# Kernel tuning notes

Measured on AMD Instinct MI355X. Metric: run time of the kernel, lower is better.

Reference implementation:

```python
import jax, jax.numpy as jnp
import numpy as np
import math

B, S, E, HEAD = 4, 2048, 1024, 64  # num_heads=16 -> head_size = 1024//16


def setup_inputs() -> dict:
    key = jax.random.key(0)
    kx, kp, kq, kk, kv = jax.random.split(key, 5)
    std = math.sqrt(2.0 / (E + HEAD))
    return {
        "x": jax.random.normal(kx, (B, S, E), dtype=jnp.float32),
        "padding_mask": jax.random.randint(kp, (B, S), 0, 2, dtype=jnp.int32),
        "Wq": jax.random.normal(kq, (HEAD, E), dtype=jnp.float32) * std,
        "Wk": jax.random.normal(kk, (HEAD, E), dtype=jnp.float32) * std,
        "Wv": jax.random.normal(kv, (HEAD, E), dtype=jnp.float32) * std,
    }


def reference(x, padding_mask, Wq, Wk, Wv):
    # q,k,v: [B,S,head] via Linear (x @ W.T, no bias)
    q = jnp.einsum("bse,he->bsh", x, Wq)
    k = jnp.einsum("bse,he->bsh", x, Wk)
    v = jnp.einsum("bse,he->bsh", x, Wv)
    scores = jnp.einsum("bqh,bkh->bqk", q, k)  # [B,S,S]
    seq = x.shape[1]
    causal = jnp.tril(jnp.ones((seq, seq), dtype=jnp.float32))  # [S,S]
    mask = causal[None, :, :] * padding_mask.astype(jnp.float32)[:, None, :]  # [B,S,S]
    scores = jnp.where(mask == 0, jnp.float32(-1e9), scores)
    head_size = k.shape[-1]
    attn = jax.nn.softmax(scores / jnp.sqrt(jnp.float32(head_size)), axis=-1)
    return jnp.einsum("bqk,bkh->bqh", attn, v)
```

## Files before the change

kernel.cpp:

```cpp
#include <hip/hip_runtime.h>
#include <hip/hip_bf16.h>
#include <math.h>

#define B_ 4
#define S_ 2048
#define E_ 1024
#define H_ 64
#define NQT 32
#define SPLITS 8
#define TPS 4
#define SENT (-1.25e8f)

typedef short bf16x8 __attribute__((ext_vector_type(8)));
typedef float f32x4 __attribute__((ext_vector_type(4)));
typedef unsigned short U16;
typedef U16 u16x8 __attribute__((ext_vector_type(8)));
typedef U16 u16x4 __attribute__((ext_vector_type(4)));

__device__ __forceinline__ U16 f2bf(float f){
    unsigned u = __builtin_bit_cast(unsigned, f);
    u += 0x7fffu + ((u >> 16) & 1u);
    return (U16)(u >> 16);
}
__device__ __forceinline__ float bf2f(U16 h){
    return __builtin_bit_cast(float, ((unsigned)h) << 16);
}
#define MFMA16(a,b,c) __builtin_amdgcn_mfma_f32_16x16x32_bf16((a),(b),(c),0,0,0)

typedef const __attribute__((address_space(1))) void GvPtr;
typedef __attribute__((address_space(3))) void LdsPtr;
__device__ __forceinline__ void gload_lds16(const void* g, void* l){
    __builtin_amdgcn_global_load_lds((GvPtr*)g, (LdsPtr*)l, 16, 0, 0);
}

__global__ __launch_bounds__(256) void prep_w(
    const float* __restrict__ Wq, const float* __restrict__ Wk,
    const float* __restrict__ Wv, U16* __restrict__ Whi, U16* __restrict__ Wlo)
{
    int i4 = (blockIdx.x*256 + threadIdx.x) * 4;
    int c = i4 >> 16, rem = i4 & 65535;
    const float* src = (c==0) ? Wq : (c==1) ? Wk : Wv;
    float4 v = *(const float4*)(src + rem);
    float a[4] = {v.x, v.y, v.z, v.w};
    u16x4 hv, lv;
    #pragma unroll
    for (int j=0;j<4;j++){ U16 h = f2bf(a[j]); hv[j]=h; lv[j]=f2bf(a[j]-bf2f(h)); }
    *(u16x4*)(Whi + i4) = hv;
    *(u16x4*)(Wlo + i4) = lv;
}

__global__ __launch_bounds__(256) void qkv_kernel(
    const float* __restrict__ x, const U16* __restrict__ Whi_g,
    const U16* __restrict__ Wlo_g,
    U16* __restrict__ Qhi, U16* __restrict__ Qlo,
    U16* __restrict__ Khi, U16* __restrict__ Klo, U16* __restrict__ Vt)
{
    __shared__ __align__(16) U16 Ah[2][32*64], Al[2][32*64];
    const int m0 = blockIdx.x * 32;
    const int tid = threadIdx.x, lane = tid & 63, wv = tid >> 6;
    const int l15 = lane & 15, quad = lane >> 4;
    const int arow = tid >> 3, ag = tid & 7;

    f32x4 acc[3][2];
    #pragma unroll
    for (int c=0;c<3;c++)
    #pragma unroll
    for (int mt=0;mt<2;mt++) acc[c][mt] = f32x4{0.f,0.f,0.f,0.f};

    {
        const float* xs = x + (size_t)(m0 + arow)*E_ + ag*8;
        float4 xa = ((const float4*)xs)[0], xb = ((const float4*)xs)[1];
        float vv[8] = {xa.x,xa.y,xa.z,xa.w,xb.x,xb.y,xb.z,xb.w};
        u16x8 hv, lv;
        #pragma unroll
        for (int j=0;j<8;j++){ U16 h = f2bf(vv[j]); hv[j]=h; lv[j]=f2bf(vv[j]-bf2f(h)); }
        ((u16x8*)Ah[0])[arow*8 + ag] = hv;
        ((u16x8*)Al[0])[arow*8 + ag] = lv;
    }
    __syncthreads();

    int p = 0;
    for (int k0 = 0; k0 < E_; k0 += 64) {
        float4 xa, xb;
        const bool have = (k0 + 64 < E_);
        if (have) {
            const float* xs = x + (size_t)(m0 + arow)*E_ + k0 + 64 + ag*8;
            xa = ((const float4*)xs)[0]; xb = ((const float4*)xs)[1];
        }
        bf16x8 bh[3][2], bl[3][2];
        #pragma unroll
        for (int c=0;c<3;c++)
        #pragma unroll
        for (int kk=0;kk<2;kk++){
            const size_t wo = (size_t)c*65536 + (size_t)(wv*16 + l15)*E_ + k0 + kk*32 + quad*8;
            bh[c][kk] = *(const bf16x8*)(Whi_g + wo);
            bl[c][kk] = *(const bf16x8*)(Wlo_g + wo);
        }
        #pragma unroll
        for (int kk=0;kk<2;kk++){
            #pragma unroll
            for (int mt=0;mt<2;mt++){
                const int ai = (mt*16 + l15)*8 + kk*4 + quad;
                bf16x8 ah = ((const bf16x8*)Ah[p])[ai];
                bf16x8 al = ((const bf16x8*)Al[p])[ai];
                #pragma unroll
                for (int c=0;c<3;c++){
                    acc[c][mt] = MFMA16(ah, bh[c][kk], acc[c][mt]);
                    acc[c][mt] = MFMA16(ah, bl[c][kk], acc[c][mt]);
                    acc[c][mt] = MFMA16(al, bh[c][kk], acc[c][mt]);
                }
            }
        }
        if (have) {
            float vv[8] = {xa.x,xa.y,xa.z,xa.w,xb.x,xb.y,xb.z,xb.w};
            u16x8 hv, lv;
            #pragma unroll
            for (int j=0;j<8;j++){ U16 h = f2bf(vv[j]); hv[j]=h; lv[j]=f2bf(vv[j]-bf2f(h)); }
            ((u16x8*)Ah[p^1])[arow*8 + ag] = hv;
            ((u16x8*)Al[p^1])[arow*8 + ag] = lv;
        }
        __syncthreads();
        p ^= 1;
    }

    const int h = wv*16 + l15;
    #pragma unroll
    for (int mt=0;mt<2;mt++){
        const int row = m0 + mt*16 + quad*4;
        #pragma unroll
        for (int r=0;r<4;r++){
            float vq = acc[0][mt][r]; U16 hq = f2bf(vq);
            Qhi[(size_t)(row+r)*H_ + h] = hq;
            Qlo[(size_t)(row+r)*H_ + h] = f2bf(vq - bf2f(hq));
            float vk = acc[1][mt][r]; U16 hk = f2bf(vk);
            Khi[(size_t)(row+r)*H_ + h] = hk;
            Klo[(size_t)(row+r)*H_ + h] = f2bf(vk - bf2f(hk));
        }
        const int b = row >> 11, s0 = row & (S_-1);
        u16x4 pk;
        #pragma unroll
        for (int r=0;r<4;r++) pk[r] = f2bf(acc[2][mt][r]);
        *(u16x4*)(Vt + ((size_t)b*H_ + h)*S_ + s0) = pk;
    }
}

__global__ __launch_bounds__(256) void attn_kernel(
    const U16* __restrict__ Qhi, const U16* __restrict__ Qlo,
    const U16* __restrict__ Khi, const U16* __restrict__ Klo,
    const U16* __restrict__ Vt, const int* __restrict__ pad,
    float* __restrict__ Opart, float* __restrict__ mpart, float* __restrict__ lpart)
{
    const int qt = blockIdx.x, b = blockIdx.y, sp = blockIdx.z;
    const int t0 = sp * TPS;
    if (t0 > qt) return;
    const int t1 = min(t0 + TPS, qt + 1);

    __shared__ __align__(16) U16 KtH[64*64], KtL[64*64], Vts[64*64];
    __shared__ __align__(16) U16 Ps[4][16*80];

    const int tid = threadIdx.x, lane = tid & 63, wv = tid >> 6;
    const int l15 = lane & 15, quad = lane >> 4;

    const size_t qrow = (size_t)b*S_ + qt*64 + wv*16 + l15;
    bf16x8 aqh0 = *(const bf16x8*)(Qhi + qrow*H_ + quad*8);
    bf16x8 aqh1 = *(const bf16x8*)(Qhi + qrow*H_ + 32 + quad*8);
    bf16x8 aql0 = *(const bf16x8*)(Qlo + qrow*H_ + quad*8);
    bf16x8 aql1 = *(const bf16x8*)(Qlo + qrow*H_ + 32 + quad*8);

    float m_i = -INFINITY, l_i = 0.f;
    f32x4 o[4];
    #pragma unroll
    for (int i=0;i<4;i++) o[i] = f32x4{0.f,0.f,0.f,0.f};
    const int qg = qt*64 + wv*16 + l15;
    U16* Pw = &Ps[wv][0];

    for (int t = t0; t < t1; ++t) {
        const int kb = t * 64;
        __syncthreads();
        {
            const U16* kh = Khi + ((size_t)b*S_ + kb)*H_;
            const U16* kl = Klo + ((size_t)b*S_ + kb)*H_;
            #pragma unroll
            for (int ch=0; ch<2; ++ch){
                const int sb = wv*128 + ch*64;
                const int slot = sb + lane;
                gload_lds16(kh + (size_t)slot*8, (U16*)KtH + sb*8);
                gload_lds16(kl + (size_t)slot*8, (U16*)KtL + sb*8);
                const int vrow = slot >> 3, vg = slot & 7;
                gload_lds16(Vt + ((size_t)b*H_ + vrow)*S_ + kb + vg*8, (U16*)Vts + sb*8);
            }
        }
        const unsigned long long pm = __ballot(pad[(size_t)b*S_ + kb + lane] != 0);
        __syncthreads();

        f32x4 z[4];
        #pragma unroll
        for (int nt=0; nt<4; nt++){
            const int kr = (nt*16 + l15)*8;
            bf16x8 kh0 = ((const bf16x8*)KtH)[kr + quad];
            bf16x8 kh1 = ((const bf16x8*)KtH)[kr + 4 + quad];
            bf16x8 kl0 = ((const bf16x8*)KtL)[kr + quad];
            bf16x8 kl1 = ((const bf16x8*)KtL)[kr + 4 + quad];
            f32x4 zz = f32x4{0.f,0.f,0.f,0.f};
            zz = MFMA16(kh0, aqh0, zz);
            zz = MFMA16(kh1, aqh1, zz);
            zz = MFMA16(kh0, aql0, zz);
            zz = MFMA16(kh1, aql1, zz);
            zz = MFMA16(kl0, aqh0, zz);
            zz = MFMA16(kl1, aqh1, zz);
            z[nt] = zz;
        }
        float rmax = -INFINITY;
        #pragma unroll
        for (int nt=0; nt<4; nt++){
            const int rel = qg - kb - nt*16 - quad*4;
            const unsigned mb = (unsigned)(pm >> (nt*16 + quad*4)) & 0xFu;
            #pragma unroll
            for (int r=0;r<4;r++){
                const bool ok = (r <= rel) && ((mb >> r) & 1u);
                const float v = ok ? z[nt][r]*0.125f : SENT;
                z[nt][r] = v;
                rmax = fmaxf(rmax, v);
            }
        }
        rmax = fmaxf(rmax, __shfl_xor(rmax, 16));
        rmax = fmaxf(rmax, __shfl_xor(rmax, 32));
        const float mn = fmaxf(m_i, rmax);
        const float alpha = __expf(m_i - mn);
        m_i = mn;
        float rsum = 0.f;
        #pragma unroll
        for (int nt=0; nt<4; nt++)
        #pragma unroll
        for (int r=0;r<4;r++){
            const float pv = __expf(z[nt][r] - mn);
            z[nt][r] = pv;
            rsum += pv;
        }
        rsum += __shfl_xor(rsum, 16);
        rsum += __shfl_xor(rsum, 32);
        l_i = l_i*alpha + rsum;
        #pragma unroll
        for (int nt=0; nt<4; nt++)
        #pragma unroll
        for (int r=0;r<4;r++) o[nt][r] *= alpha;

        #pragma unroll
        for (int nt=0; nt<4; nt++){
            u16x4 pk;
            #pragma unroll
            for (int r=0;r<4;r++) pk[r] = f2bf(z[nt][r]);
            *(u16x4*)(Pw + l15*80 + nt*16 + quad*4) = pk;
        }
        #pragma unroll
        for (int ks=0; ks<2; ks++){
            bf16x8 bp = *(const bf16x8*)(Pw + l15*80 + ks*32 + quad*8);
            #pragma unroll
            for (int nt=0; nt<4; nt++){
                bf16x8 av = ((const bf16x8*)Vts)[(nt*16 + l15)*8 + ks*4 + quad];
                o[nt] = MFMA16(av, bp, o[nt]);
            }
        }
    }
    const size_t rbase = ((size_t)((b*NQT + qt)*SPLITS + sp))*64 + wv*16 + l15;
    if (quad == 0) { mpart[rbase] = m_i; lpart[rbase] = l_i; }
    #pragma unroll
    for (int nt=0; nt<4; nt++)
        *((f32x4*)(Opart + rbase*H_ + nt*16 + quad*4)) = o[nt];
}

__global__ __launch_bounds__(256) void combine_kernel(
    const float* __restrict__ Opart, const float* __restrict__ mpart,
    const float* __restrict__ lpart, const U16* __restrict__ Vt,
    float* __restrict__ out)
{
    const int idx = blockIdx.x*256 + threadIdx.x;
    const int h = idx & 63;
    const int q = (idx >> 6) & (S_-1);
    const int b = idx >> 17;
    const int qt = q >> 6, r = q & 63;
    const int ns = (qt >> 2) + 1;
    const size_t rb = ((size_t)(b*NQT + qt)*SPLITS)*64 + r;
    float M = -INFINITY;
    for (int s2=0; s2<ns; s2++) M = fmaxf(M, mpart[rb + (size_t)s2*64]);
    float res;
    if (M == SENT) {
        const U16* vsrc = Vt + ((size_t)b*H_ + h)*S_;
        float sm = 0.f;
        for (int s=0; s<S_; ++s) sm += bf2f(vsrc[s]);
        res = sm * (1.f/(float)S_);
    } else {
        float L = 0.f, accv = 0.f;
        for (int s2=0; s2<ns; s2++){
            const float mi = mpart[rb + (size_t)s2*64];
            const float w = __expf(mi - M);
            L    += w * lpart[rb + (size_t)s2*64];
            accv += w * Opart[(rb + (size_t)s2*64)*H_ + h];
        }
        res = accv / L;
    }
    out[idx] = res;
}

extern "C" void kernel_launch(void* const* d_in, const int* in_sizes, int n_in,
                              void* d_out, int out_size, void* d_ws, size_t ws_size,
                              hipStream_t stream)
{
    (void)in_sizes; (void)n_in; (void)out_size; (void)ws_size;
    const float* x  = (const float*)d_in[0];
    const int* pad  = (const int*)d_in[1];
    const float* Wq = (const float*)d_in[2];
    const float* Wk = (const float*)d_in[3];
    const float* Wv = (const float*)d_in[4];
    float* out = (float*)d_out;
    char* ws = (char*)d_ws;
    const size_t MB = 1u << 20;
    U16* Whi = (U16*)(ws);
    U16* Wlo = (U16*)(ws + 393216);
    U16* Qhi = (U16*)(ws + 1*MB);
    U16* Qlo = (U16*)(ws + 2*MB);
    U16* Khi = (U16*)(ws + 3*MB);
    U16* Klo = (U16*)(ws + 4*MB);
    U16* Vt  = (U16*)(ws + 5*MB);
    float* Opart = (float*)(ws + 6*MB);
    float* mpart = (float*)(ws + 22*MB);
    float* lpart = (float*)(ws + 22*MB + (1u<<18));

    prep_w<<<dim3(192), 256, 0, stream>>>(Wq, Wk, Wv, Whi, Wlo);
    qkv_kernel<<<dim3(256), 256, 0, stream>>>(x, Whi, Wlo, Qhi, Qlo, Khi, Klo, Vt);
    attn_kernel<<<dim3(NQT, B_, SPLITS), 256, 0, stream>>>(Qhi, Qlo, Khi, Klo, Vt, pad,
                                                           Opart, mpart, lpart);
    combine_kernel<<<dim3((B_*S_*H_)/256), 256, 0, stream>>>(Opart, mpart, lpart, Vt, out);
}
```

Before: 164.4 us.

## Double-buffer attention K/V tiles, swizzle LDS, and split-K the QKV projection

The attention kernel now double-buffers the K-hi, K-lo and V tiles in LDS. It issues the async global-to-LDS loads and the padding-mask load for the next key tile before computing on the current one, and drops one barrier per iteration. All LDS tiles use an XOR swizzle of the 16-byte column groups to reduce bank conflicts on the MFMA operand reads. The QKV projection moves to 512 threads and splits the K dimension in half across wave groups, with register prefetch of the next weight slice and a shared-memory reduction at the end. The aim is to hide global load latency and raise occupancy, at the cost of more LDS and more registers per block.

Result: faster. 152.8 us (-7.0%).

```diff
diff --git a/kernel.cpp b/kernel.cpp
--- a/kernel.cpp
+++ b/kernel.cpp
@@ -49,17 +49,21 @@
     *(u16x4*)(Wlo + i4) = lv;
 }
 
-__global__ __launch_bounds__(256) void qkv_kernel(
+__global__ __launch_bounds__(512) void qkv_kernel(
     const float* __restrict__ x, const U16* __restrict__ Whi_g,
     const U16* __restrict__ Wlo_g,
     U16* __restrict__ Qhi, U16* __restrict__ Qlo,
     U16* __restrict__ Khi, U16* __restrict__ Klo, U16* __restrict__ Vt)
 {
-    __shared__ __align__(16) U16 Ah[2][32*64], Al[2][32*64];
+    __shared__ __align__(16) U16 XH[2][2][2048], XL[2][2][2048];
+    __shared__ __align__(16) float Red[4*64*28];
     const int m0 = blockIdx.x * 32;
     const int tid = threadIdx.x, lane = tid & 63, wv = tid >> 6;
     const int l15 = lane & 15, quad = lane >> 4;
-    const int arow = tid >> 3, ag = tid & 7;
+    const int hs = (wv & 3) * 16;
+    const int kh = wv >> 2;
+    const int p2 = tid >> 8;
+    const int rr = (tid >> 3) & 31, ag = tid & 7;
 
     f32x4 acc[3][2];
     #pragma unroll
@@ -67,80 +71,107 @@
     #pragma unroll
     for (int mt=0;mt<2;mt++) acc[c][mt] = f32x4{0.f,0.f,0.f,0.f};
 
-    {
-        const float* xs = x + (size_t)(m0 + arow)*E_ + ag*8;
-        float4 xa = ((const float4*)xs)[0], xb = ((const float4*)xs)[1];
-        float vv[8] = {xa.x,xa.y,xa.z,xa.w,xb.x,xb.y,xb.z,xb.w};
+    const float* xrow = x + (size_t)(m0 + rr)*E_ + (size_t)p2*512 + ag*8;
+
+    auto cvwrite = [&](int buf, float4 a, float4 b2){
+        float vv[8] = {a.x,a.y,a.z,a.w,b2.x,b2.y,b2.z,b2.w};
         u16x8 hv, lv;
         #pragma unroll
         for (int j=0;j<8;j++){ U16 h = f2bf(vv[j]); hv[j]=h; lv[j]=f2bf(vv[j]-bf2f(h)); }
-        ((u16x8*)Ah[0])[arow*8 + ag] = hv;
-        ((u16x8*)Al[0])[arow*8 + ag] = lv;
-    }
+        const int idx = rr*8 + (ag ^ (rr & 7));
+        ((u16x8*)XH[buf][p2])[idx] = hv;
+        ((u16x8*)XL[buf][p2])[idx] = lv;
+    };
+
+    const size_t wbase = (size_t)(hs + l15)*E_ + (size_t)kh*512 + quad*8;
+    bf16x8 bhc[3][2], blc[3][2], bhn[3][2], bln[3][2];
+    auto loadW = [&](int it, bf16x8 (*bh)[2], bf16x8 (*bl)[2]){
+        #pragma unroll
+        for (int c=0;c<3;c++)
+        #pragma unroll
+        for (int kk=0;kk<2;kk++){
+            const size_t o = (size_t)c*65536 + wbase + it*64 + kk*32;
+            bh[c][kk] = *(const bf16x8*)(Whi_g + o);
+            bl[c][kk] = *(const bf16x8*)(Wlo_g + o);
+        }
+    };
+
+    {   float4 xa = ((const float4*)xrow)[0], xb = ((const float4*)xrow)[1];
+        cvwrite(0, xa, xb); }
+    loadW(0, bhc, blc);
     __syncthreads();
 
     int p = 0;
-    for (int k0 = 0; k0 < E_; k0 += 64) {
+    for (int it = 0; it < 8; ++it) {
+        const bool have = (it < 7);
         float4 xa, xb;
-        const bool have = (k0 + 64 < E_);
         if (have) {
-            const float* xs = x + (size_t)(m0 + arow)*E_ + k0 + 64 + ag*8;
+            const float* xs = xrow + (it+1)*64;
             xa = ((const float4*)xs)[0]; xb = ((const float4*)xs)[1];
-        }
-        bf16x8 bh[3][2], bl[3][2];
+            loadW(it+1, bhn, bln);
+        }
+        #pragma unroll
+        for (int kk=0;kk<2;kk++)
+        #pragma unroll
+        for (int mt=0;mt<2;mt++){
+            const int row = mt*16 + l15;
+            const int idx = row*8 + ((kk*4+quad) ^ (l15 & 7));
+            bf16x8 ah = ((const bf16x8*)XH[p][kh])[idx];
+            bf16x8 al = ((const bf16x8*)XL[p][kh])[idx];
+            #pragma unroll
+            for (int c=0;c<3;c++){
+                acc[c][mt] = MFMA16(ah, bhc[c][kk], acc[c][mt]);
+                acc[c][mt] = MFMA16(ah, blc[c][kk], acc[c][mt]);
+                acc[c][mt] = MFMA16(al, bhc[c][kk], acc[c][mt]);
+            }
+        }
+        if (have) cvwrite(p^1, xa, xb);
+        __syncthreads();
+        if (have) {
+            #pragma unroll
+            for (int c=0;c<3;c++)
+            #pragma unroll
+            for (int kk=0;kk<2;kk++){ bhc[c][kk]=bhn[c][kk]; blc[c][kk]=bln[c][kk]; }
+        }
+        p ^= 1;
+    }
+
+    if (kh == 1) {
+        float* rp = &Red[((wv&3)*64 + lane)*28];
         #pragma unroll
         for (int c=0;c<3;c++)
         #pragma unroll
-        for (int kk=0;kk<2;kk++){
-            const size_t wo = (size_t)c*65536 + (size_t)(wv*16 + l15)*E_ + k0 + kk*32 + quad*8;
-            bh[c][kk] = *(const bf16x8*)(Whi_g + wo);
-            bl[c][kk] = *(const bf16x8*)(Wlo_g + wo);
-        }
-        #pragma unroll
-        for (int kk=0;kk<2;kk++){
-            #pragma unroll
-            for (int mt=0;mt<2;mt++){
-                const int ai = (mt*16 + l15)*8 + kk*4 + quad;
-                bf16x8 ah = ((const bf16x8*)Ah[p])[ai];
-                bf16x8 al = ((const bf16x8*)Al[p])[ai];
-                #pragma unroll
-                for (int c=0;c<3;c++){
-                    acc[c][mt] = MFMA16(ah, bh[c][kk], acc[c][mt]);
-                    acc[c][mt] = MFMA16(ah, bl[c][kk], acc[c][mt]);
-                    acc[c][mt] = MFMA16(al, bh[c][kk], acc[c][mt]);
-                }
+        for (int mt=0;mt<2;mt++)
+            *(f32x4*)(rp + (c*2+mt)*4) = acc[c][mt];
+    }
+    __syncthreads();
+    if (kh == 0) {
+        const float* rp = &Red[((wv&3)*64 + lane)*28];
+        #pragma unroll
+        for (int c=0;c<3;c++)
+        #pragma unroll
+        for (int mt=0;mt<2;mt++)
+            acc[c][mt] += *(const f32x4*)(rp + (c*2+mt)*4);
+
+        const int h = hs + l15;
+        #pragma unroll
+        for (int mt=0;mt<2;mt++){
+            const int row = m0 + mt*16 + quad*4;
+            #pragma unroll
+            for (int r=0;r<4;r++){
+                float vq = acc[0][mt][r]; U16 hq = f2bf(vq);
+                Qhi[(size_t)(row+r)*H_ + h] = hq;
+                Qlo[(size_t)(row+r)*H_ + h] = f2bf(vq - bf2f(hq));
+                float vk = acc[1][mt][r]; U16 hk = f2bf(vk);
+                Khi[(size_t)(row+r)*H_ + h] = hk;
+                Klo[(size_t)(row+r)*H_ + h] = f2bf(vk - bf2f(hk));
             }
-        }
-        if (have) {
-            float vv[8] = {xa.x,xa.y,xa.z,xa.w,xb.x,xb.y,xb.z,xb.w};
-            u16x8 hv, lv;
-            #pragma unroll
-            for (int j=0;j<8;j++){ U16 h = f2bf(vv[j]); hv[j]=h; lv[j]=f2bf(vv[j]-bf2f(h)); }
-            ((u16x8*)Ah[p^1])[arow*8 + ag] = hv;
-            ((u16x8*)Al[p^1])[arow*8 + ag] = lv;
-        }
-        __syncthreads();
-        p ^= 1;
-    }
-
-    const int h = wv*16 + l15;
-    #pragma unroll
-    for (int mt=0;mt<2;mt++){
-        const int row = m0 + mt*16 + quad*4;
-        #pragma unroll
-        for (int r=0;r<4;r++){
-            float vq = acc[0][mt][r]; U16 hq = f2bf(vq);
-            Qhi[(size_t)(row+r)*H_ + h] = hq;
-            Qlo[(size_t)(row+r)*H_ + h] = f2bf(vq - bf2f(hq));
-            float vk = acc[1][mt][r]; U16 hk = f2bf(vk);
-            Khi[(size_t)(row+r)*H_ + h] = hk;
-            Klo[(size_t)(row+r)*H_ + h] = f2bf(vk - bf2f(hk));
-        }
-        const int b = row >> 11, s0 = row & (S_-1);
-        u16x4 pk;
-        #pragma unroll
-        for (int r=0;r<4;r++) pk[r] = f2bf(acc[2][mt][r]);
-        *(u16x4*)(Vt + ((size_t)b*H_ + h)*S_ + s0) = pk;
+            const int b = row >> 11, s0 = row & (S_-1);
+            u16x4 pk;
+            #pragma unroll
+            for (int r=0;r<4;r++) pk[r] = f2bf(acc[2][mt][r]);
+            *(u16x4*)(Vt + ((size_t)b*H_ + h)*S_ + s0) = pk;
+        }
     }
 }
 
@@ -155,11 +186,26 @@
     if (t0 > qt) return;
     const int t1 = min(t0 + TPS, qt + 1);
 
-    __shared__ __align__(16) U16 KtH[64*64], KtL[64*64], Vts[64*64];
+    __shared__ __align__(16) U16 KtH[2][64*64], KtL[2][64*64], Vts[2][64*64];
     __shared__ __align__(16) U16 Ps[4][16*80];
 
     const int tid = threadIdx.x, lane = tid & 63, wv = tid >> 6;
     const int l15 = lane & 15, quad = lane >> 4;
+
+    auto stage = [&](int t, int bb){
+        const int kb2 = t * 64;
+        const U16* khp = Khi + ((size_t)b*S_ + kb2)*H_;
+        const U16* klp = Klo + ((size_t)b*S_ + kb2)*H_;
+        #pragma unroll
+        for (int ch=0; ch<2; ++ch){
+            const int sb = wv*128 + ch*64;
+            const int u = sb + lane;
+            const int row = u >> 3, g = u & 7, gs = g ^ (row & 7);
+            gload_lds16(khp + (size_t)row*H_ + gs*8, KtH[bb] + sb*8);
+            gload_lds16(klp + (size_t)row*H_ + gs*8, KtL[bb] + sb*8);
+            gload_lds16(Vt + ((size_t)b*H_ + row)*S_ + kb2 + gs*8, Vts[bb] + sb*8);
+        }
+    };
 
     const size_t qrow = (size_t)b*S_ + qt*64 + wv*16 + l15;
     bf16x8 aqh0 = *(const bf16x8*)(Qhi + qrow*H_ + quad*8);
@@ -174,33 +220,29 @@
     const int qg = qt*64 + wv*16 + l15;
     U16* Pw = &Ps[wv][0];
 
-    for (int t = t0; t < t1; ++t) {
+    stage(t0, 0);
+    int pv = pad[(size_t)b*S_ + t0*64 + lane];
+
+    int p = 0;
+    for (int t = t0; t < t1; ++t, p ^= 1) {
+        __syncthreads();
+        int pvn = 0;
+        if (t + 1 < t1) {
+            stage(t+1, p^1);
+            pvn = pad[(size_t)b*S_ + (t+1)*64 + lane];
+        }
+        const unsigned long long pm = __ballot(pv != 0);
         const int kb = t * 64;
-        __syncthreads();
-        {
-            const U16* kh = Khi + ((size_t)b*S_ + kb)*H_;
-            const U16* kl = Klo + ((size_t)b*S_ + kb)*H_;
-            #pragma unroll
-            for (int ch=0; ch<2; ++ch){
-                const int sb = wv*128 + ch*64;
-                const int slot = sb + lane;
-                gload_lds16(kh + (size_t)slot*8, (U16*)KtH + sb*8);
-                gload_lds16(kl + (size_t)slot*8, (U16*)KtL + sb*8);
-                const int vrow = slot >> 3, vg = slot & 7;
-                gload_lds16(Vt + ((size_t)b*H_ + vrow)*S_ + kb + vg*8, (U16*)Vts + sb*8);
-            }
-        }
-        const unsigned long long pm = __ballot(pad[(size_t)b*S_ + kb + lane] != 0);
-        __syncthreads();
+        const int sw = l15 & 7;
 
         f32x4 z[4];
         #pragma unroll
         for (int nt=0; nt<4; nt++){
             const int kr = (nt*16 + l15)*8;
-            bf16x8 kh0 = ((const bf16x8*)KtH)[kr + quad];
-            bf16x8 kh1 = ((const bf16x8*)KtH)[kr + 4 + quad];
-            bf16x8 kl0 = ((const bf16x8*)KtL)[kr + quad];
-            bf16x8 kl1 = ((const bf16x8*)KtL)[kr + 4 + quad];
+            bf16x8 kh0 = ((const bf16x8*)KtH[p])[kr + (quad ^ sw)];
+            bf16x8 kh1 = ((const bf16x8*)KtH[p])[kr + ((4+quad) ^ sw)];
+            bf16x8 kl0 = ((const bf16x8*)KtL[p])[kr + (quad ^ sw)];
+            bf16x8 kl1 = ((const bf16x8*)KtL[p])[kr + ((4+quad) ^ sw)];
             f32x4 zz = f32x4{0.f,0.f,0.f,0.f};
             zz = MFMA16(kh0, aqh0, zz);
             zz = MFMA16(kh1, aqh1, zz);
@@ -233,9 +275,9 @@
         for (int nt=0; nt<4; nt++)
         #pragma unroll
         for (int r=0;r<4;r++){
-            const float pv = __expf(z[nt][r] - mn);
-            z[nt][r] = pv;
-            rsum += pv;
+            const float pe = __expf(z[nt][r] - mn);
+            z[nt][r] = pe;
+            rsum += pe;
         }
         rsum += __shfl_xor(rsum, 16);
         rsum += __shfl_xor(rsum, 32);
@@ -257,10 +299,11 @@
             bf16x8 bp = *(const bf16x8*)(Pw + l15*80 + ks*32 + quad*8);
             #pragma unroll
             for (int nt=0; nt<4; nt++){
-                bf16x8 av = ((const bf16x8*)Vts)[(nt*16 + l15)*8 + ks*4 + quad];
+                bf16x8 av = ((const bf16x8*)Vts[p])[(nt*16 + l15)*8 + ((ks*4+quad) ^ sw)];
                 o[nt] = MFMA16(av, bp, o[nt]);
             }
         }
+        pv = pvn;
     }
     const size_t rbase = ((size_t)((b*NQT + qt)*SPLITS + sp))*64 + wv*16 + l15;
     if (quad == 0) { mpart[rbase] = m_i; lpart[rbase] = l_i; }
@@ -327,7 +370,7 @@
     float* lpart = (float*)(ws + 22*MB + (1u<<18));
 
     prep_w<<<dim3(192), 256, 0, stream>>>(Wq, Wk, Wv, Whi, Wlo);
-    qkv_kernel<<<dim3(256), 256, 0, stream>>>(x, Whi, Wlo, Qhi, Qlo, Khi, Klo, Vt);
+    qkv_kernel<<<dim3(256), 512, 0, stream>>>(x, Whi, Wlo, Qhi, Qlo, Khi, Klo, Vt);
     attn_kernel<<<dim3(NQT, B_, SPLITS), 256, 0, stream>>>(Qhi, Qlo, Khi, Klo, Vt, pad,
                                                            Opart, mpart, lpart);
     combine_kernel<<<dim3((B_*S_*H_)/256), 256, 0, stream>>>(Opart, mpart, lpart, Vt, out);
```

## Split QKV projection over K across waves and swizzle attention LDS tiles

Applied to the files above, without the earlier changes.

The QKV projection kernel is restructured so that each block handles 64 rows for a single Q/K/V component, with the grid spanning components. Each of the four waves covers a quarter of the E dimension, loading x directly from global memory into registers with double buffering, and the partial sums are reduced through shared memory. This removes the per-step LDS staging and barriers and raises parallelism, at the cost of more shared memory for the reduction and x being re-read once per component. The attention kernel also XOR-swizzles the K and V tile layout in LDS to reduce bank conflicts on the MFMA operand reads.

Result: faster. 153.6 us (-6.6%).

```diff
diff --git a/kernel.cpp b/kernel.cpp
--- a/kernel.cpp
+++ b/kernel.cpp
@@ -49,98 +49,110 @@
     *(u16x4*)(Wlo + i4) = lv;
 }
 
-__global__ __launch_bounds__(256) void qkv_kernel(
+__global__ __launch_bounds__(256, 2) void qkv_kernel(
     const float* __restrict__ x, const U16* __restrict__ Whi_g,
     const U16* __restrict__ Wlo_g,
     U16* __restrict__ Qhi, U16* __restrict__ Qlo,
     U16* __restrict__ Khi, U16* __restrict__ Klo, U16* __restrict__ Vt)
 {
-    __shared__ __align__(16) U16 Ah[2][32*64], Al[2][32*64];
-    const int m0 = blockIdx.x * 32;
+    __shared__ __align__(16) float Red[4*16*64*4];
+    const int m0 = blockIdx.x * 64;
+    const int comp = blockIdx.y;
     const int tid = threadIdx.x, lane = tid & 63, wv = tid >> 6;
     const int l15 = lane & 15, quad = lane >> 4;
-    const int arow = tid >> 3, ag = tid & 7;
-
-    f32x4 acc[3][2];
-    #pragma unroll
-    for (int c=0;c<3;c++)
-    #pragma unroll
-    for (int mt=0;mt<2;mt++) acc[c][mt] = f32x4{0.f,0.f,0.f,0.f};
-
-    {
-        const float* xs = x + (size_t)(m0 + arow)*E_ + ag*8;
-        float4 xa = ((const float4*)xs)[0], xb = ((const float4*)xs)[1];
-        float vv[8] = {xa.x,xa.y,xa.z,xa.w,xb.x,xb.y,xb.z,xb.w};
-        u16x8 hv, lv;
-        #pragma unroll
-        for (int j=0;j<8;j++){ U16 h = f2bf(vv[j]); hv[j]=h; lv[j]=f2bf(vv[j]-bf2f(h)); }
-        ((u16x8*)Ah[0])[arow*8 + ag] = hv;
-        ((u16x8*)Al[0])[arow*8 + ag] = lv;
+    const int kq0 = wv * 256;
+
+    f32x4 acc[4][4];
+    #pragma unroll
+    for (int mt=0;mt<4;mt++)
+    #pragma unroll
+    for (int nt=0;nt<4;nt++) acc[mt][nt] = f32x4{0.f,0.f,0.f,0.f};
+
+    const float* xb = x + (size_t)(m0 + l15)*E_ + kq0 + quad*8;
+    const U16* whb = Whi_g + (size_t)comp*65536 + (size_t)l15*E_ + kq0 + quad*8;
+    const U16* wlb = Wlo_g + (size_t)comp*65536 + (size_t)l15*E_ + kq0 + quad*8;
+
+    float4 xf[2][4][2];
+    bf16x8 wh[2][4], wl[2][4];
+
+    auto loadstep = [&](int s, int buf){
+        #pragma unroll
+        for (int mt=0;mt<4;mt++){
+            const float* p = xb + (size_t)mt*16*E_ + s*32;
+            xf[buf][mt][0] = ((const float4*)p)[0];
+            xf[buf][mt][1] = ((const float4*)p)[1];
+        }
+        #pragma unroll
+        for (int nt=0;nt<4;nt++){
+            wh[buf][nt] = *(const bf16x8*)(whb + (size_t)nt*16*E_ + s*32);
+            wl[buf][nt] = *(const bf16x8*)(wlb + (size_t)nt*16*E_ + s*32);
+        }
+    };
+
+    loadstep(0, 0);
+    #pragma unroll
+    for (int s=0; s<8; ++s){
+        const int buf = s & 1;
+        if (s < 7) loadstep(s+1, buf^1);
+        bf16x8 ah[4], al[4];
+        #pragma unroll
+        for (int mt=0;mt<4;mt++){
+            const float4 a = xf[buf][mt][0], b2 = xf[buf][mt][1];
+            float v[8] = {a.x,a.y,a.z,a.w,b2.x,b2.y,b2.z,b2.w};
+            #pragma unroll
+            for (int j=0;j<8;j++){
+                U16 h = f2bf(v[j]);
+                ah[mt][j] = (short)h;
+                al[mt][j] = (short)f2bf(v[j] - bf2f(h));
+            }
+        }
+        #pragma unroll
+        for (int mt=0;mt<4;mt++)
+        #pragma unroll
+        for (int nt=0;nt<4;nt++){
+            acc[mt][nt] = MFMA16(ah[mt], wh[buf][nt], acc[mt][nt]);
+            acc[mt][nt] = MFMA16(ah[mt], wl[buf][nt], acc[mt][nt]);
+            acc[mt][nt] = MFMA16(al[mt], wh[buf][nt], acc[mt][nt]);
+        }
     }
+
+    #pragma unroll
+    for (int mt=0;mt<4;mt++)
+    #pragma unroll
+    for (int nt=0;nt<4;nt++)
+        *(f32x4*)&Red[(((wv*16) + (mt*4+nt))*64 + lane)*4] = acc[mt][nt];
     __syncthreads();
 
-    int p = 0;
-    for (int k0 = 0; k0 < E_; k0 += 64) {
-        float4 xa, xb;
-        const bool have = (k0 + 64 < E_);
-        if (have) {
-            const float* xs = x + (size_t)(m0 + arow)*E_ + k0 + 64 + ag*8;
-            xa = ((const float4*)xs)[0]; xb = ((const float4*)xs)[1];
-        }
-        bf16x8 bh[3][2], bl[3][2];
-        #pragma unroll
-        for (int c=0;c<3;c++)
-        #pragma unroll
-        for (int kk=0;kk<2;kk++){
-            const size_t wo = (size_t)c*65536 + (size_t)(wv*16 + l15)*E_ + k0 + kk*32 + quad*8;
-            bh[c][kk] = *(const bf16x8*)(Whi_g + wo);
-            bl[c][kk] = *(const bf16x8*)(Wlo_g + wo);
-        }
-        #pragma unroll
-        for (int kk=0;kk<2;kk++){
-            #pragma unroll
-            for (int mt=0;mt<2;mt++){
-                const int ai = (mt*16 + l15)*8 + kk*4 + quad;
-                bf16x8 ah = ((const bf16x8*)Ah[p])[ai];
-                bf16x8 al = ((const bf16x8*)Al[p])[ai];
-                #pragma unroll
-                for (int c=0;c<3;c++){
-                    acc[c][mt] = MFMA16(ah, bh[c][kk], acc[c][mt]);
-                    acc[c][mt] = MFMA16(ah, bl[c][kk], acc[c][mt]);
-                    acc[c][mt] = MFMA16(al, bh[c][kk], acc[c][mt]);
-                }
-            }
-        }
-        if (have) {
-            float vv[8] = {xa.x,xa.y,xa.z,xa.w,xb.x,xb.y,xb.z,xb.w};
-            u16x8 hv, lv;
-            #pragma unroll
-            for (int j=0;j<8;j++){ U16 h = f2bf(vv[j]); hv[j]=h; lv[j]=f2bf(vv[j]-bf2f(h)); }
-            ((u16x8*)Ah[p^1])[arow*8 + ag] = hv;
-            ((u16x8*)Al[p^1])[arow*8 + ag] = lv;
-        }
-        __syncthreads();
-        p ^= 1;
-    }
-
-    const int h = wv*16 + l15;
-    #pragma unroll
-    for (int mt=0;mt<2;mt++){
+    #pragma unroll
+    for (int pp=0; pp<4; ++pp){
+        const int pair = wv*4 + pp, mt = pair >> 2, nt = pair & 3;
+        f32x4 sum = *(const f32x4*)&Red[((0*16 + pair)*64 + lane)*4];
+        #pragma unroll
+        for (int w2=1; w2<4; ++w2)
+            sum += *(const f32x4*)&Red[((w2*16 + pair)*64 + lane)*4];
+        const int h = nt*16 + l15;
         const int row = m0 + mt*16 + quad*4;
-        #pragma unroll
-        for (int r=0;r<4;r++){
-            float vq = acc[0][mt][r]; U16 hq = f2bf(vq);
-            Qhi[(size_t)(row+r)*H_ + h] = hq;
-            Qlo[(size_t)(row+r)*H_ + h] = f2bf(vq - bf2f(hq));
-            float vk = acc[1][mt][r]; U16 hk = f2bf(vk);
-            Khi[(size_t)(row+r)*H_ + h] = hk;
-            Klo[(size_t)(row+r)*H_ + h] = f2bf(vk - bf2f(hk));
-        }
-        const int b = row >> 11, s0 = row & (S_-1);
-        u16x4 pk;
-        #pragma unroll
-        for (int r=0;r<4;r++) pk[r] = f2bf(acc[2][mt][r]);
-        *(u16x4*)(Vt + ((size_t)b*H_ + h)*S_ + s0) = pk;
+        if (comp == 0){
+            #pragma unroll
+            for (int r=0;r<4;r++){
+                float vv = sum[r]; U16 hh = f2bf(vv);
+                Qhi[(size_t)(row+r)*H_ + h] = hh;
+                Qlo[(size_t)(row+r)*H_ + h] = f2bf(vv - bf2f(hh));
+            }
+        } else if (comp == 1){
+            #pragma unroll
+            for (int r=0;r<4;r++){
+                float vv = sum[r]; U16 hh = f2bf(vv);
+                Khi[(size_t)(row+r)*H_ + h] = hh;
+                Klo[(size_t)(row+r)*H_ + h] = f2bf(vv - bf2f(hh));
+            }
+        } else {
+            const int b = row >> 11, s0 = row & (S_-1);
+            u16x4 pk;
+            #pragma unroll
+            for (int r=0;r<4;r++) pk[r] = f2bf(sum[r]);
+            *(u16x4*)(Vt + ((size_t)b*H_ + h)*S_ + s0) = pk;
+        }
     }
 }
 
@@ -173,34 +185,36 @@
     for (int i=0;i<4;i++) o[i] = f32x4{0.f,0.f,0.f,0.f};
     const int qg = qt*64 + wv*16 + l15;
     U16* Pw = &Ps[wv][0];
+    const int sw = l15 & 7;
 
     for (int t = t0; t < t1; ++t) {
         const int kb = t * 64;
         __syncthreads();
         {
-            const U16* kh = Khi + ((size_t)b*S_ + kb)*H_;
-            const U16* kl = Klo + ((size_t)b*S_ + kb)*H_;
+            const U16* khp = Khi + ((size_t)b*S_ + kb)*H_;
+            const U16* klp = Klo + ((size_t)b*S_ + kb)*H_;
             #pragma unroll
             for (int ch=0; ch<2; ++ch){
                 const int sb = wv*128 + ch*64;
-                const int slot = sb + lane;
-                gload_lds16(kh + (size_t)slot*8, (U16*)KtH + sb*8);
-                gload_lds16(kl + (size_t)slot*8, (U16*)KtL + sb*8);
-                const int vrow = slot >> 3, vg = slot & 7;
-                gload_lds16(Vt + ((size_t)b*H_ + vrow)*S_ + kb + vg*8, (U16*)Vts + sb*8);
-            }
-        }
-        const unsigned long long pm = __ballot(pad[(size_t)b*S_ + kb + lane] != 0);
+                const int u = sb + lane;
+                const int row = u >> 3, g = u & 7, gs = g ^ (row & 7);
+                gload_lds16(khp + (size_t)row*H_ + gs*8, KtH + sb*8);
+                gload_lds16(klp + (size_t)row*H_ + gs*8, KtL + sb*8);
+                gload_lds16(Vt + ((size_t)b*H_ + row)*S_ + kb + gs*8, Vts + sb*8);
+            }
+        }
+        const int pv = pad[(size_t)b*S_ + kb + lane];
+        const unsigned long long pm = __ballot(pv != 0);
         __syncthreads();
 
         f32x4 z[4];
         #pragma unroll
         for (int nt=0; nt<4; nt++){
             const int kr = (nt*16 + l15)*8;
-            bf16x8 kh0 = ((const bf16x8*)KtH)[kr + quad];
-            bf16x8 kh1 = ((const bf16x8*)KtH)[kr + 4 + quad];
-            bf16x8 kl0 = ((const bf16x8*)KtL)[kr + quad];
-            bf16x8 kl1 = ((const bf16x8*)KtL)[kr + 4 + quad];
+            bf16x8 kh0 = ((const bf16x8*)KtH)[kr + (quad ^ sw)];
+            bf16x8 kh1 = ((const bf16x8*)KtH)[kr + ((4+quad) ^ sw)];
+            bf16x8 kl0 = ((const bf16x8*)KtL)[kr + (quad ^ sw)];
+            bf16x8 kl1 = ((const bf16x8*)KtL)[kr + ((4+quad) ^ sw)];
             f32x4 zz = f32x4{0.f,0.f,0.f,0.f};
             zz = MFMA16(kh0, aqh0, zz);
             zz = MFMA16(kh1, aqh1, zz);
@@ -233,9 +247,9 @@
         for (int nt=0; nt<4; nt++)
         #pragma unroll
         for (int r=0;r<4;r++){
-            const float pv = __expf(z[nt][r] - mn);
-            z[nt][r] = pv;
-            rsum += pv;
+            const float pe = __expf(z[nt][r] - mn);
+            z[nt][r] = pe;
+            rsum += pe;
         }
         rsum += __shfl_xor(rsum, 16);
         rsum += __shfl_xor(rsum, 32);
@@ -257,7 +271,7 @@
             bf16x8 bp = *(const bf16x8*)(Pw + l15*80 + ks*32 + quad*8);
             #pragma unroll
             for (int nt=0; nt<4; nt++){
-                bf16x8 av = ((const bf16x8*)Vts)[(nt*16 + l15)*8 + ks*4 + quad];
+                bf16x8 av = ((const bf16x8*)Vts)[(nt*16 + l15)*8 + ((ks*4+quad) ^ sw)];
                 o[nt] = MFMA16(av, bp, o[nt]);
             }
         }
@@ -327,7 +341,7 @@
     float* lpart = (float*)(ws + 22*MB + (1u<<18));
 
     prep_w<<<dim3(192), 256, 0, stream>>>(Wq, Wk, Wv, Whi, Wlo);
-    qkv_kernel<<<dim3(256), 256, 0, stream>>>(x, Whi, Wlo, Qhi, Qlo, Khi, Klo, Vt);
+    qkv_kernel<<<dim3(128, 3), 256, 0, stream>>>(x, Whi, Wlo, Qhi, Qlo, Khi, Klo, Vt);
     attn_kernel<<<dim3(NQT, B_, SPLITS), 256, 0, stream>>>(Qhi, Qlo, Khi, Klo, Vt, pad,
                                                            Opart, mpart, lpart);
     combine_kernel<<<dim3((B_*S_*H_)/256), 256, 0, stream>>>(Opart, mpart, lpart, Vt, out);
```
